# Kernel tuning notes

Measured on AMD Instinct MI355X. Metric: run time of the kernel, lower is better.

The kernel has to match this reference:

```python
import jax, jax.numpy as jnp
import numpy as np

IMAGE_SIZE = 256
PSIZE = 6
STRIDE = 2
WINDOW = IMAGE_SIZE + 1 - PSIZE  # 251
CUR = np.arange(0, WINDOW, STRIDE)
if CUR[-1] != WINDOW - 1:
    CUR = np.concatenate([CUR, np.array([WINDOW - 1])])
NPOS = len(CUR)  # 126 strided window positions per axis
BATCH = 128


def setup_inputs() -> dict:
    key = jax.random.key(0)
    x = jax.random.normal(key, (BATCH, 1, IMAGE_SIZE, IMAGE_SIZE), dtype=jnp.float32)
    return {"x": x}


def reference(x):
    # Equivalent to patch_tf.forward(to_patch): for each strided window position
    # (r, c) in CUR x CUR and each in-patch offset (i, j) in [0, PSIZE)^2,
    # output[b, r*NPOS + c, i*PSIZE + j] = x[b, 0, r + i, c + j].
    cur = jnp.asarray(CUR, dtype=jnp.int32)          # [NPOS]
    off = jnp.arange(PSIZE, dtype=jnp.int32)         # [PSIZE]
    row_idx = cur[:, None] + off[None, :]            # [NPOS, PSIZE]
    col_idx = cur[:, None] + off[None, :]            # [NPOS, PSIZE]
    img = x[:, 0]                                    # [B, H, W]
    # Advanced-index gather -> [B, NPOS, NPOS, PSIZE, PSIZE]
    patches = img[:, row_idx[:, None, :, None], col_idx[None, :, None, :]]
    return patches.reshape(x.shape[0], NPOS * NPOS, PSIZE * PSIZE)
```

## Files before the change

### kernel.cpp

```cpp
#include <hip/hip_runtime.h>


#define IMG 256
#define PSZ 6
#define NPOS 126
#define BATCHN 128
#define NB 4
#define NGROUPS 32
#define TROWS (2 * NB + 4)
#define VECS_PER_BAND 1134

typedef float fvec4 __attribute__((ext_vector_type(4)));

__global__ __launch_bounds__(256) void image2patch_kernel(
    const float* __restrict__ x, float* __restrict__ out) {
  __shared__ float tile[TROWS * IMG];

  const int blk = blockIdx.x;
  const int b = blk >> 5;
  const int g = blk & 31;
  const int i0 = g * NB;
  const int t = threadIdx.x;

  const float* src = x + (size_t)b * (IMG * IMG);
  for (int idx = t; idx < TROWS * (IMG / 4); idx += 256) {
    const int row  = idx >> 6;
    const int col4 = idx & 63;
    const int grow = 2 * i0 + row;
    if (grow < IMG) {
      fvec4 v = reinterpret_cast<const fvec4*>(src + (size_t)grow * IMG)[col4];
      reinterpret_cast<fvec4*>(&tile[row * IMG])[col4] = v;
    }
  }
  __syncthreads();

  for (int band = 0; band < NB; ++band) {
    const int i = i0 + band;
    if (i >= NPOS) break;
    fvec4* outp = reinterpret_cast<fvec4*>(
        out + ((size_t)b * (NPOS * NPOS) + (size_t)i * NPOS) * (PSZ * PSZ));
    const int rbase = 2 * band;
    for (int q = t; q < VECS_PER_BAND; q += 256) {
      const int f  = q * 4;
      const int j  = f / 36;
      const int k0 = f - j * 36;
      const int col = 2 * j;
      fvec4 v;
      { const int k = k0;     const int r = k / PSZ, c = k - PSZ * r; v.x = tile[(rbase + r) * IMG + col + c]; }
      { const int k = k0 + 1; const int r = k / PSZ, c = k - PSZ * r; v.y = tile[(rbase + r) * IMG + col + c]; }
      { const int k = k0 + 2; const int r = k / PSZ, c = k - PSZ * r; v.z = tile[(rbase + r) * IMG + col + c]; }
      { const int k = k0 + 3; const int r = k / PSZ, c = k - PSZ * r; v.w = tile[(rbase + r) * IMG + col + c]; }
      __builtin_nontemporal_store(v, &outp[q]);
    }
  }
}

extern "C" void kernel_launch(void* const* d_in, const int* in_sizes, int n_in,
                              void* d_out, int out_size, void* d_ws, size_t ws_size,
                              hipStream_t stream) {
  const float* x = (const float*)d_in[0];
  float* out = (float*)d_out;
  image2patch_kernel<<<BATCHN * NGROUPS, 256, 0, stream>>>(x, out);
}
```

Baseline: 324.1 us.

## Use 6 bands per block, padded LDS tile, and precomputed gather offsets

After: 319.8 us. No clear change (-1.3%).

```diff
diff --git a/kernel.cpp b/kernel.cpp
--- a/kernel.cpp
+++ b/kernel.cpp
@@ -5,52 +5,65 @@
 #define PSZ 6
 #define NPOS 126
 #define BATCHN 128
-#define NB 4
-#define NGROUPS 32
-#define TROWS (2 * NB + 4)
+#define NB 6
+#define NGROUPS 21
+#define TROWS 16
+#define LDSW 257
 #define VECS_PER_BAND 1134
+#define NITER 5
 
 typedef float fvec4 __attribute__((ext_vector_type(4)));
 
 __global__ __launch_bounds__(256) void image2patch_kernel(
     const float* __restrict__ x, float* __restrict__ out) {
-  __shared__ float tile[TROWS * IMG];
+  __shared__ float tile[TROWS * LDSW];
 
   const int blk = blockIdx.x;
-  const int b = blk >> 5;
-  const int g = blk & 31;
+  const int b = blk / NGROUPS;
+  const int g = blk - b * NGROUPS;
   const int i0 = g * NB;
   const int t = threadIdx.x;
 
-  const float* src = x + (size_t)b * (IMG * IMG);
-  for (int idx = t; idx < TROWS * (IMG / 4); idx += 256) {
-    const int row  = idx >> 6;
-    const int col4 = idx & 63;
-    const int grow = 2 * i0 + row;
-    if (grow < IMG) {
-      fvec4 v = reinterpret_cast<const fvec4*>(src + (size_t)grow * IMG)[col4];
-      reinterpret_cast<fvec4*>(&tile[row * IMG])[col4] = v;
+  const float* src = x + (size_t)b * (IMG * IMG) + (size_t)(12 * g) * IMG;
+  #pragma unroll
+  for (int w = 0; w < TROWS; ++w) {
+    tile[w * LDSW + t] = src[w * IMG + t];
+  }
+
+  int off[NITER][4];
+  #pragma unroll
+  for (int n = 0; n < NITER; ++n) {
+    const int q = t + n * 256;
+    const int j = q / 9;
+    const int s = q - 9 * j;
+    const int k0 = 4 * s;
+    #pragma unroll
+    for (int m = 0; m < 4; ++m) {
+      const int k = k0 + m;
+      const int r = k / PSZ;
+      const int c = k - PSZ * r;
+      off[n][m] = r * LDSW + 2 * j + c;
     }
   }
+
   __syncthreads();
 
+  #pragma unroll
   for (int band = 0; band < NB; ++band) {
-    const int i = i0 + band;
-    if (i >= NPOS) break;
+    const float* tb = &tile[(2 * band) * LDSW];
     fvec4* outp = reinterpret_cast<fvec4*>(
-        out + ((size_t)b * (NPOS * NPOS) + (size_t)i * NPOS) * (PSZ * PSZ));
-    const int rbase = 2 * band;
-    for (int q = t; q < VECS_PER_BAND; q += 256) {
-      const int f  = q * 4;
-      const int j  = f / 36;
-      const int k0 = f - j * 36;
-      const int col = 2 * j;
-      fvec4 v;
-      { const int k = k0;     const int r = k / PSZ, c = k - PSZ * r; v.x = tile[(rbase + r) * IMG + col + c]; }
-      { const int k = k0 + 1; const int r = k / PSZ, c = k - PSZ * r; v.y = tile[(rbase + r) * IMG + col + c]; }
-      { const int k = k0 + 2; const int r = k / PSZ, c = k - PSZ * r; v.z = tile[(rbase + r) * IMG + col + c]; }
-      { const int k = k0 + 3; const int r = k / PSZ, c = k - PSZ * r; v.w = tile[(rbase + r) * IMG + col + c]; }
-      __builtin_nontemporal_store(v, &outp[q]);
+        out + ((size_t)b * (NPOS * NPOS) + (size_t)(i0 + band) * NPOS) * (PSZ * PSZ));
+    #pragma unroll
+    for (int n = 0; n < NITER; ++n) {
+      const int q = t + n * 256;
+      if (q < VECS_PER_BAND) {
+        fvec4 v;
+        v.x = tb[off[n][0]];
+        v.y = tb[off[n][1]];
+        v.z = tb[off[n][2]];
+        v.w = tb[off[n][3]];
+        outp[q] = v;
+      }
     }
   }
 }
```
